# Optimization experiments

Measured on AMD Instinct MI355X. Metric: run time of the kernel, lower is better.

## Reference

```python
import jax, jax.numpy as jnp
import numpy as np

# bior3.5 analysis filters (pywt conventions, dec_len = 12).
# dec_lo derived from the CDF(3,5) construction: sqrt(2)/2048 * conv([1,5,10,10,5,1], [-20,160,-524,832,-524,160,-20])
# matches pywt: [-0.0138107, 0.0414420, 0.0524806, -0.2679272, -0.0718155, 0.9667476, ...] (symmetric)
_DEC_LO = jnp.asarray(
    np.array([-20., 60., 76., -388., -104., 1400., 1400., -104., -388., 76., 60., -20.]) * np.sqrt(2.0) / 2048.0,
    dtype=jnp.float32)
# dec_hi = QMF of rec_lo = sqrt(2)*[1,3,3,1]/8, zero-padded to length 12 as pywt stores it (phase matters for periodization)
_DEC_HI = jnp.asarray(
    np.array([0., 0., 0., 0., -1., 3., -3., 1., 0., 0., 0., 0.]) * np.sqrt(2.0) / 8.0,
    dtype=jnp.float32)


def _dwt_last(x, f):
    # pywt mode='periodization' along last axis: out[i] = sum_j f[j] * x[(2i+1-j) mod N], N even -> length N//2.
    # Equivalent to wrap-padding F-2 on the left, then stride-2 valid correlation with reversed filter.
    F = f.shape[0]
    N = x.shape[-1]
    xp = jnp.concatenate([x[..., N - (F - 2):], x], axis=-1)  # [..., N+F-2]
    lhs = xp.reshape(-1, 1, xp.shape[-1])
    rhs = f[::-1].astype(x.dtype).reshape(1, 1, F)
    out = jax.lax.conv_general_dilated(lhs, rhs, window_strides=(2,), padding='VALID')  # [M,1,N//2]
    return out.reshape(*x.shape[:-1], N // 2)


def _dwt_axis(x, f, axis):
    x = jnp.swapaxes(x, axis, -1)
    return jnp.swapaxes(_dwt_last(x, f), axis, -1)


def _dwt2(x):
    # separable 2D DWT over the last two axes; pywt dwt2 keys: 'aa','da','ad','dd' (first letter = axis -2)
    lo = _dwt_axis(x, _DEC_LO, -1)
    hi = _dwt_axis(x, _DEC_HI, -1)
    aa = _dwt_axis(lo, _DEC_LO, -2)  # cA
    da = _dwt_axis(lo, _DEC_HI, -2)  # cH
    ad = _dwt_axis(hi, _DEC_LO, -2)  # cV
    dd = _dwt_axis(hi, _DEC_HI, -2)  # cD
    return aa, (da, ad, dd)


def _forward(x, k):
    # wavedec2 to level k; the torch module stacks 3 channels (we carry them as a batch-like dim)
    # and concatenates (cH, cV, cD) along dim 0 for each level, coarsest level first.
    a = x
    highs = []
    for _ in range(k):
        a, (da, ad, dd) = _dwt2(a)
        highs.insert(0, jnp.concatenate([da, ad, dd], axis=0))  # [3B, 3, h, w]
    return (a, *highs)


def setup_inputs() -> dict:
    key = jax.random.key(0)
    x = jax.random.normal(key, (8, 3, 1024, 1024), dtype=jnp.float32)
    return {"x": x, "k": 3}


def reference(x, k):
    return _forward(x, k)
```

## Files before the change

kernel.cpp:

```cpp
#include <hip/hip_runtime.h>


#define OW 32
#define OH 16
#define IN_ROWS (2 * OH + 10)
#define IN_COLS_P 80
#define TR_PAD 44

__global__ __launch_bounds__(256, 6) void dwt2_level(
    const float* __restrict__ src, int N,
    float* __restrict__ aa, float* __restrict__ da,
    float* __restrict__ ad, float* __restrict__ dd)
{
    constexpr float SQ2 = 1.41421356237309504880f;
    constexpr float c_lo[12] = {
        -20.f * SQ2 / 2048.f,  60.f * SQ2 / 2048.f,   76.f * SQ2 / 2048.f,
        -388.f * SQ2 / 2048.f, -104.f * SQ2 / 2048.f, 1400.f * SQ2 / 2048.f,
        1400.f * SQ2 / 2048.f, -104.f * SQ2 / 2048.f, -388.f * SQ2 / 2048.f,
        76.f * SQ2 / 2048.f,   60.f * SQ2 / 2048.f,   -20.f * SQ2 / 2048.f };
    constexpr float c_hi4[4] = { -SQ2 / 8.f, 3.f * SQ2 / 8.f, -3.f * SQ2 / 8.f, SQ2 / 8.f };

    const int h    = N >> 1;
    const int mask = N - 1;
    const int bc   = blockIdx.z;
    const int j0   = blockIdx.x * OW;
    const int i0   = blockIdx.y * OH;
    const int tid  = threadIdx.x;

    __shared__ float s_in[IN_ROWS][IN_COLS_P];
    __shared__ float s_loT[OW][TR_PAD];
    __shared__ float s_hiT[OW][TR_PAD];

    const float* img = src + (unsigned)bc * (unsigned)(N * N);
    const int r0 = 2 * i0 - 10;
    const int c0 = 2 * j0 - 12;

    const bool interior = (r0 >= 0) && (r0 + IN_ROWS <= N) &&
                          (c0 >= 0) && (c0 + IN_COLS_P <= N);

    if (interior) {
        #pragma unroll
        for (int t = tid; t < IN_ROWS * 20; t += 256) {
            int r = t / 20;
            int q = t - r * 20;
            float4 v = *(const float4*)(img + (unsigned)((r0 + r) * N + c0 + 4 * q));
            *(float4*)&s_in[r][4 * q] = v;
        }
    } else {
        for (int t = tid; t < IN_ROWS * IN_COLS_P; t += 256) {
            int r = t / IN_COLS_P;
            int c = t - r * IN_COLS_P;
            int gr = (r0 + r) & mask;
            int gc = (c0 + c) & mask;
            s_in[r][c] = img[(unsigned)(gr * N + gc)];
        }
    }
    __syncthreads();

    #pragma unroll
    for (int t = tid; t < IN_ROWS * 16; t += 256) {
        int r = t >> 4;
        int m = t & 15;
        const float* p = &s_in[r][4 * m];
        float v[16];
        *(float4*)&v[0]  = *(const float4*)&p[0];
        *(float4*)&v[4]  = *(const float4*)&p[4];
        *(float4*)&v[8]  = *(const float4*)&p[8];
        *(float4*)&v[12] = *(const float4*)&p[12];
        float lo0 = 0.f, lo1 = 0.f;
        #pragma unroll
        for (int jc = 0; jc < 12; ++jc) {
            lo0 += c_lo[jc] * v[13 - jc];
            lo1 += c_lo[jc] * v[15 - jc];
        }
        float hi0 = 0.f, hi1 = 0.f;
        #pragma unroll
        for (int k = 0; k < 4; ++k) {
            hi0 += c_hi4[k] * v[9 - k];
            hi1 += c_hi4[k] * v[11 - k];
        }
        s_loT[2 * m + 0][r] = lo0;
        s_loT[2 * m + 1][r] = lo1;
        s_hiT[2 * m + 0][r] = hi0;
        s_hiT[2 * m + 1][r] = hi1;
    }
    __syncthreads();

    const int tx = tid & 31;
    const int ty = tid >> 5;
    float l[16], hh[16];
    {
        const float* pl = &s_loT[tx][4 * ty];
        const float* ph = &s_hiT[tx][4 * ty];
        *(float4*)&l[0]   = *(const float4*)&pl[0];
        *(float4*)&l[4]   = *(const float4*)&pl[4];
        *(float4*)&l[8]   = *(const float4*)&pl[8];
        *(float4*)&l[12]  = *(const float4*)&pl[12];
        *(float4*)&hh[0]  = *(const float4*)&ph[0];
        *(float4*)&hh[4]  = *(const float4*)&ph[4];
        *(float4*)&hh[8]  = *(const float4*)&ph[8];
        *(float4*)&hh[12] = *(const float4*)&ph[12];
    }
    float vaa0 = 0.f, vad0 = 0.f, vaa1 = 0.f, vad1 = 0.f;
    #pragma unroll
    for (int jr = 0; jr < 12; ++jr) {
        vaa0 += c_lo[jr] * l[11 - jr];
        vaa1 += c_lo[jr] * l[13 - jr];
        vad0 += c_lo[jr] * hh[11 - jr];
        vad1 += c_lo[jr] * hh[13 - jr];
    }
    float vda0 = 0.f, vdd0 = 0.f, vda1 = 0.f, vdd1 = 0.f;
    #pragma unroll
    for (int k = 0; k < 4; ++k) {
        vda0 += c_hi4[k] * l[7 - k];
        vda1 += c_hi4[k] * l[9 - k];
        vdd0 += c_hi4[k] * hh[7 - k];
        vdd1 += c_hi4[k] * hh[9 - k];
    }
    const unsigned ob = (unsigned)((bc * h + i0 + 2 * ty) * h + j0 + tx);
    const unsigned oh = (unsigned)h;
    aa[ob] = vaa0;  aa[ob + oh] = vaa1;
    da[ob] = vda0;  da[ob + oh] = vda1;
    ad[ob] = vad0;  ad[ob + oh] = vad1;
    dd[ob] = vdd0;  dd[ob + oh] = vdd1;
}

extern "C" void kernel_launch(void* const* d_in, const int* in_sizes, int n_in,
                              void* d_out, int out_size, void* d_ws, size_t ws_size,
                              hipStream_t stream) {
    const float* x = (const float*)d_in[0];
    float* out = (float*)d_out;
    float* ws  = (float*)d_ws;

    const size_t s512 = (size_t)24 * 512 * 512;
    const size_t s256 = (size_t)24 * 256 * 256;
    const size_t s128 = (size_t)24 * 128 * 128;

    float* a_out = out;
    float* h3 = out + s128;
    float* h2 = out + 4 * s128;
    float* h1 = out + 4 * s128 + 3 * s256;

    float* aa1 = ws;
    float* aa2 = ws + s512;
    (void)in_sizes; (void)n_in; (void)out_size; (void)ws_size;

    dim3 blk(256, 1, 1);
    dwt2_level<<<dim3(512 / OW, 512 / OH, 24), blk, 0, stream>>>(
        x, 1024, aa1, h1, h1 + s512, h1 + 2 * s512);
    dwt2_level<<<dim3(256 / OW, 256 / OH, 24), blk, 0, stream>>>(
        aa1, 512, aa2, h2, h2 + s256, h2 + 2 * s256);
    dwt2_level<<<dim3(128 / OW, 128 / OH, 24), blk, 0, stream>>>(
        aa2, 256, a_out, h3, h3 + s128, h3 + 2 * s128);
}
```

Baseline: 93.10 us.

## Fuse row filtering into global loads, drop input shared tile, template on N

The input shared-memory tile and its barrier are removed. Each thread now reads 20 contiguous floats straight from global memory (float4 when not wrapping) and computes four row-filter outputs in registers before writing the transposed lo/hi tiles. The kernel is templated on image size so masks and strides become constants, and the occupancy hint rises from 6 to 8. The cost is overlapping global reads between neighbouring threads, which now go through cache rather than shared memory, and a possibly non-16-byte-aligned float2 transpose layout.

```diff
diff --git a/kernel.cpp b/kernel.cpp
--- a/kernel.cpp
+++ b/kernel.cpp
@@ -4,11 +4,11 @@
 #define OW 32
 #define OH 16
 #define IN_ROWS (2 * OH + 10)
-#define IN_COLS_P 80
-#define TR_PAD 44
+#define TRS 42
 
-__global__ __launch_bounds__(256, 6) void dwt2_level(
-    const float* __restrict__ src, int N,
+template <int N>
+__global__ __launch_bounds__(256, 8) void dwt2_level(
+    const float* __restrict__ src,
     float* __restrict__ aa, float* __restrict__ da,
     float* __restrict__ ad, float* __restrict__ dd)
 {
@@ -20,88 +20,61 @@
         76.f * SQ2 / 2048.f,   60.f * SQ2 / 2048.f,   -20.f * SQ2 / 2048.f };
     constexpr float c_hi4[4] = { -SQ2 / 8.f, 3.f * SQ2 / 8.f, -3.f * SQ2 / 8.f, SQ2 / 8.f };
 
-    const int h    = N >> 1;
-    const int mask = N - 1;
-    const int bc   = blockIdx.z;
-    const int j0   = blockIdx.x * OW;
-    const int i0   = blockIdx.y * OH;
-    const int tid  = threadIdx.x;
+    constexpr int h    = N >> 1;
+    constexpr int mask = N - 1;
 
-    __shared__ float s_in[IN_ROWS][IN_COLS_P];
-    __shared__ float s_loT[OW][TR_PAD];
-    __shared__ float s_hiT[OW][TR_PAD];
+    const int bc  = blockIdx.z;
+    const int j0  = blockIdx.x * OW;
+    const int i0  = blockIdx.y * OH;
+    const int tid = threadIdx.x;
+
+    __shared__ float s_loT[OW][TRS];
+    __shared__ float s_hiT[OW][TRS];
 
     const float* img = src + (unsigned)bc * (unsigned)(N * N);
     const int r0 = 2 * i0 - 10;
     const int c0 = 2 * j0 - 12;
 
-    const bool interior = (r0 >= 0) && (r0 + IN_ROWS <= N) &&
-                          (c0 >= 0) && (c0 + IN_COLS_P <= N);
-
-    if (interior) {
+    for (int t = tid; t < IN_ROWS * (OW / 4); t += 256) {
+        const int m = t & (OW / 4 - 1);
+        const int r = t >> 3;
+        const int gr = (r0 + r) & mask;
+        const float* row = img + (unsigned)(gr * N);
+        const int cb = c0 + 8 * m;
+        float v[20];
+        if (cb >= 0) {
+            #pragma unroll
+            for (int q = 0; q < 5; ++q)
+                *(float4*)&v[4 * q] = *(const float4*)&row[cb + 4 * q];
+        } else {
+            #pragma unroll
+            for (int k = 0; k < 20; ++k)
+                v[k] = row[(cb + k) & mask];
+        }
         #pragma unroll
-        for (int t = tid; t < IN_ROWS * 20; t += 256) {
-            int r = t / 20;
-            int q = t - r * 20;
-            float4 v = *(const float4*)(img + (unsigned)((r0 + r) * N + c0 + 4 * q));
-            *(float4*)&s_in[r][4 * q] = v;
+        for (int d = 0; d < 4; ++d) {
+            float lo = 0.f, hi = 0.f;
+            #pragma unroll
+            for (int jc = 0; jc < 12; ++jc)
+                lo += c_lo[jc] * v[2 * d + 13 - jc];
+            #pragma unroll
+            for (int k = 0; k < 4; ++k)
+                hi += c_hi4[k] * v[2 * d + 9 - k];
+            s_loT[4 * m + d][r] = lo;
+            s_hiT[4 * m + d][r] = hi;
         }
-    } else {
-        for (int t = tid; t < IN_ROWS * IN_COLS_P; t += 256) {
-            int r = t / IN_COLS_P;
-            int c = t - r * IN_COLS_P;
-            int gr = (r0 + r) & mask;
-            int gc = (c0 + c) & mask;
-            s_in[r][c] = img[(unsigned)(gr * N + gc)];
-        }
-    }
-    __syncthreads();
-
-    #pragma unroll
-    for (int t = tid; t < IN_ROWS * 16; t += 256) {
-        int r = t >> 4;
-        int m = t & 15;
-        const float* p = &s_in[r][4 * m];
-        float v[16];
-        *(float4*)&v[0]  = *(const float4*)&p[0];
-        *(float4*)&v[4]  = *(const float4*)&p[4];
-        *(float4*)&v[8]  = *(const float4*)&p[8];
-        *(float4*)&v[12] = *(const float4*)&p[12];
-        float lo0 = 0.f, lo1 = 0.f;
-        #pragma unroll
-        for (int jc = 0; jc < 12; ++jc) {
-            lo0 += c_lo[jc] * v[13 - jc];
-            lo1 += c_lo[jc] * v[15 - jc];
-        }
-        float hi0 = 0.f, hi1 = 0.f;
-        #pragma unroll
-        for (int k = 0; k < 4; ++k) {
-            hi0 += c_hi4[k] * v[9 - k];
-            hi1 += c_hi4[k] * v[11 - k];
-        }
-        s_loT[2 * m + 0][r] = lo0;
-        s_loT[2 * m + 1][r] = lo1;
-        s_hiT[2 * m + 0][r] = hi0;
-        s_hiT[2 * m + 1][r] = hi1;
     }
     __syncthreads();
 
     const int tx = tid & 31;
     const int ty = tid >> 5;
-    float l[16], hh[16];
-    {
-        const float* pl = &s_loT[tx][4 * ty];
-        const float* ph = &s_hiT[tx][4 * ty];
-        *(float4*)&l[0]   = *(const float4*)&pl[0];
-        *(float4*)&l[4]   = *(const float4*)&pl[4];
-        *(float4*)&l[8]   = *(const float4*)&pl[8];
-        *(float4*)&l[12]  = *(const float4*)&pl[12];
-        *(float4*)&hh[0]  = *(const float4*)&ph[0];
-        *(float4*)&hh[4]  = *(const float4*)&ph[4];
-        *(float4*)&hh[8]  = *(const float4*)&ph[8];
-        *(float4*)&hh[12] = *(const float4*)&ph[12];
+    float l[14], hh[14];
+    #pragma unroll
+    for (int e = 0; e < 7; ++e) {
+        *(float2*)&l[2 * e]  = *(const float2*)&s_loT[tx][4 * ty + 2 * e];
+        *(float2*)&hh[2 * e] = *(const float2*)&s_hiT[tx][4 * ty + 2 * e];
     }
-    float vaa0 = 0.f, vad0 = 0.f, vaa1 = 0.f, vad1 = 0.f;
+    float vaa0 = 0.f, vaa1 = 0.f, vad0 = 0.f, vad1 = 0.f;
     #pragma unroll
     for (int jr = 0; jr < 12; ++jr) {
         vaa0 += c_lo[jr] * l[11 - jr];
@@ -109,7 +82,7 @@
         vad0 += c_lo[jr] * hh[11 - jr];
         vad1 += c_lo[jr] * hh[13 - jr];
     }
-    float vda0 = 0.f, vdd0 = 0.f, vda1 = 0.f, vdd1 = 0.f;
+    float vda0 = 0.f, vda1 = 0.f, vdd0 = 0.f, vdd1 = 0.f;
     #pragma unroll
     for (int k = 0; k < 4; ++k) {
         vda0 += c_hi4[k] * l[7 - k];
@@ -118,11 +91,10 @@
         vdd1 += c_hi4[k] * hh[9 - k];
     }
     const unsigned ob = (unsigned)((bc * h + i0 + 2 * ty) * h + j0 + tx);
-    const unsigned oh = (unsigned)h;
-    aa[ob] = vaa0;  aa[ob + oh] = vaa1;
-    da[ob] = vda0;  da[ob + oh] = vda1;
-    ad[ob] = vad0;  ad[ob + oh] = vad1;
-    dd[ob] = vdd0;  dd[ob + oh] = vdd1;
+    aa[ob] = vaa0;  aa[ob + h] = vaa1;
+    da[ob] = vda0;  da[ob + h] = vda1;
+    ad[ob] = vad0;  ad[ob + h] = vad1;
+    dd[ob] = vdd0;  dd[ob + h] = vdd1;
 }
 
 extern "C" void kernel_launch(void* const* d_in, const int* in_sizes, int n_in,
@@ -146,10 +118,10 @@
     (void)in_sizes; (void)n_in; (void)out_size; (void)ws_size;
 
     dim3 blk(256, 1, 1);
-    dwt2_level<<<dim3(512 / OW, 512 / OH, 24), blk, 0, stream>>>(
-        x, 1024, aa1, h1, h1 + s512, h1 + 2 * s512);
-    dwt2_level<<<dim3(256 / OW, 256 / OH, 24), blk, 0, stream>>>(
-        aa1, 512, aa2, h2, h2 + s256, h2 + 2 * s256);
-    dwt2_level<<<dim3(128 / OW, 128 / OH, 24), blk, 0, stream>>>(
-        aa2, 256, a_out, h3, h3 + s128, h3 + 2 * s128);
+    dwt2_level<1024><<<dim3(512 / OW, 512 / OH, 24), blk, 0, stream>>>(
+        x, aa1, h1, h1 + s512, h1 + 2 * s512);
+    dwt2_level<512><<<dim3(256 / OW, 256 / OH, 24), blk, 0, stream>>>(
+        aa1, aa2, h2, h2 + s256, h2 + 2 * s256);
+    dwt2_level<256><<<dim3(128 / OW, 128 / OH, 24), blk, 0, stream>>>(
+        aa2, a_out, h3, h3 + s128, h3 + 2 * s128);
 }
```

After: 233.2 us. 150% more time.
